# Kernel optimization log

Measured on AMD Instinct MI355X. Metric: run time of the kernel, lower is better.

The kernel has to match this reference:

```python
import jax, jax.numpy as jnp
import numpy as np
from jax import lax


def _conv(x, w, pad):
    # NCHW / OIHW conv, stride 1
    return lax.conv_general_dilated(
        x, w, window_strides=(1, 1), padding=((pad, pad), (pad, pad)),
        dimension_numbers=("NCHW", "OIHW", "NCHW"))


def setup_inputs() -> dict:
    key = jax.random.key(0)
    k1, k2, k3, k4 = jax.random.split(key, 4)
    B, C, H, W = 16, 64, 128, 128
    OUT = 64
    x = jax.random.normal(k1, (B, C, H, W), jnp.float32)
    w_off = jax.random.normal(k2, (2 * C, C, 3, 3), jnp.float32) * 0.01  # offset conv, init std 0.01
    w_conv = jax.random.normal(k3, (OUT, C, 3, 3), jnp.float32) * 0.05
    b_conv = jax.random.normal(k4, (OUT,), jnp.float32) * 0.01
    return {"x": x, "w_off": w_off, "w_conv": w_conv, "b_conv": b_conv}


def _deform(x, w_off):
    B, C, H, W = x.shape
    off = _conv(x, w_off, 1)                      # (B, 2C, H, W)
    # Faithful to torch .view(-1, H, W, 2): raw row-major memory reinterpretation
    off = off.reshape(B * C, H * W, 2)            # (BC, HW, 2) -> (row_off, col_off)
    gr, gc = jnp.meshgrid(jnp.arange(H), jnp.arange(W), indexing="ij")
    grid = jnp.stack([gr.reshape(-1), gc.reshape(-1)], -1).astype(x.dtype)  # (HW, 2)
    coords = off + grid                           # (BC, HW, 2)
    rows = jnp.clip(coords[..., 0], 0, H - 1)
    cols = jnp.clip(coords[..., 1], 0, W - 1)
    r0 = jnp.floor(rows); r1 = jnp.ceil(rows)
    c0 = jnp.floor(cols); c1 = jnp.ceil(cols)
    xf = x.reshape(B * C, H * W)

    def gather(r, c):
        idx = lax.stop_gradient((r * W + c).astype(jnp.int32))
        return jnp.take_along_axis(xf, idx, axis=1)

    v_lt = gather(r0, c0)   # (floor row, floor col)
    v_rb = gather(r1, c1)   # (ceil row,  ceil col)
    v_lb = gather(r0, c1)   # (floor row, ceil col)
    v_rt = gather(r1, c0)   # (ceil row,  floor col)
    fr = rows - r0
    fc = cols - c0
    vals_t = fr * (v_rt - v_lt) + v_lt
    vals_b = fr * (v_rb - v_lb) + v_lb
    mapped = fc * (vals_b - vals_t) + vals_t      # (BC, HW)
    return mapped.reshape(B, C, H, W)


def reference(x, w_off, w_conv, b_conv):
    xd = _deform(x, w_off)
    return _conv(xd, w_conv, 1) + b_conv[None, :, None, None]
```

## Files before the change

kernel.cpp:

```cpp
#include <hip/hip_runtime.h>

typedef _Float16 f16;
typedef _Float16 half8 __attribute__((ext_vector_type(8)));
typedef _Float16 f16x2 __attribute__((ext_vector_type(2)));
typedef float f32x4 __attribute__((ext_vector_type(4)));
typedef int i32x4 __attribute__((ext_vector_type(4)));
typedef unsigned short ushort_t;


__global__ __launch_bounds__(256) void pack_w_k(
    const float* __restrict__ w_off, const float* __restrict__ w_conv,
    f16* __restrict__ W1p, f16* __restrict__ W2p)
{
    int t = blockIdx.x * 256 + threadIdx.x;
    if (t < 73728) {
        int tap = t >> 13, oc = (t >> 6) & 127, ic = t & 63;
        W1p[t] = (f16)w_off[(oc * 64 + ic) * 9 + tap];
    } else {
        int t2 = t - 73728;
        int tap = t2 >> 12, oc = (t2 >> 6) & 63, ic = t2 & 63;
        W2p[t2] = (f16)w_conv[(oc * 64 + ic) * 9 + tap];
    }
}

__global__ __launch_bounds__(256) void transpose_k(
    const float* __restrict__ x, f16* __restrict__ xT)
{
    __shared__ float lds[64 * 132];
    const int b = blockIdx.x >> 7, h = blockIdx.x & 127;
    const int tid = threadIdx.x;
    const float4* x4 = (const float4*)x;
    for (int i = tid; i < 2048; i += 256) {
        int ic = i >> 5, wq = i & 31;
        float4 v = x4[(b * 64 + ic) * 4096 + h * 32 + wq];
        *(float4*)&lds[ic * 132 + wq * 4] = v;
    }
    __syncthreads();
    for (int i = tid; i < 1024; i += 256) {
        int w = i & 127, kg = i >> 7;
        half8 hv;
        #pragma unroll
        for (int j = 0; j < 8; ++j) hv[j] = (f16)lds[(kg * 8 + j) * 132 + w];
        *(half8*)&xT[(((size_t)(b * 128 + h) * 128 + w) << 6) + kg * 8] = hv;
    }
}

__device__ __forceinline__ float bilin(const float* __restrict__ xp, float rr, float cc) {
    rr = fminf(fmaxf(rr, 0.f), 127.f);
    cc = fminf(fmaxf(cc, 0.f), 127.f);
    const float r0f = floorf(rr), c0f = floorf(cc);
    const float r1f = ceilf(rr),  c1f = ceilf(cc);
    const int r0 = (int)r0f, r1 = (int)r1f, c0 = (int)c0f, c1 = (int)c1f;
    const float v_lt = xp[(r0 << 7) + c0];
    const float v_rt = xp[(r1 << 7) + c0];
    const float v_lb = xp[(r0 << 7) + c1];
    const float v_rb = xp[(r1 << 7) + c1];
    const float fr = rr - r0f, fc = cc - c0f;
    const float vt = fr * (v_rt - v_lt) + v_lt;
    const float vb = fr * (v_rb - v_lb) + v_lb;
    return fc * (vb - vt) + vt;
}

__global__ __launch_bounds__(256, 2) void conv1_deform_k(
    const f16* __restrict__ xT, const float* __restrict__ x,
    const f16* __restrict__ Wp, f16* __restrict__ mapped)
{
    __shared__ char lds[66560];
    ushort_t* cres = (ushort_t*)lds;

    const int tid = threadIdx.x;
    const int t = blockIdx.x;
    const int b = blockIdx.y;

    {
        const i32x4* s4 = (const i32x4*)xT;
        for (int s = tid; s < 4160; s += 256) {
            int kg = s & 7, q = s >> 3;
            int c = q % 130, r = q / 130;
            int rowg = 2 * t + r - 1, wg = c - 1;
            i32x4 v = {0, 0, 0, 0};
            if ((unsigned)rowg < 128u && (unsigned)wg < 128u)
                v = s4[((b * 128 + rowg) * 128 + wg) * 8 + kg];
            int off = (q << 7) + (kg << 4);
            off ^= (c & 7) << 4;
            *(i32x4*)(lds + off) = v;
        }
    }
    __syncthreads();

    const int lane = tid & 63, wv = tid >> 6;
    const int l15 = lane & 15, l4 = lane >> 4;
    const int wm = wv >> 1, u = wv & 1;
    const int ocbA = wm * 64 + l15;

    f32x4 acc[4][8];
    #pragma unroll
    for (int m = 0; m < 4; ++m)
        #pragma unroll
        for (int n = 0; n < 8; ++n) acc[m][n] = {0.f, 0.f, 0.f, 0.f};

    half8 a_cur[4], a_nxt[4];
    #pragma unroll
    for (int m = 0; m < 4; ++m)
        a_cur[m] = *(const half8*)&Wp[(0 * 128 + ocbA + m * 16) * 64 + l4 * 8];

    #pragma unroll
    for (int step = 0; step < 18; ++step) {
        const int tap = step >> 1, ks = step & 1;
        const int ky = tap / 3, kx = tap % 3;
        if (step < 17) {
            const int tap1 = (step + 1) >> 1, ks1 = (step + 1) & 1;
            #pragma unroll
            for (int m = 0; m < 4; ++m)
                a_nxt[m] = *(const half8*)&Wp[(tap1 * 128 + ocbA + m * 16) * 64 + ks1 * 32 + l4 * 8];
        }
        half8 bf[8];
        #pragma unroll
        for (int n = 0; n < 8; ++n) {
            const int c = n * 16 + l15 + kx;
            int off = (((u + ky) * 130 + c) << 7) + (ks << 6) + (l4 << 4);
            off ^= (c & 7) << 4;
            bf[n] = *(const half8*)(lds + off);
        }
        #pragma unroll
        for (int m = 0; m < 4; ++m)
            #pragma unroll
            for (int n = 0; n < 8; ++n)
                acc[m][n] = __builtin_amdgcn_mfma_f32_16x16x32_f16(
                    a_cur[m], bf[n], acc[m][n], 0, 0, 0);
        #pragma unroll
        for (int m = 0; m < 4; ++m) a_cur[m] = a_nxt[m];
    }

    __syncthreads();

    #pragma unroll
    for (int m = 0; m < 4; ++m) {
        const int oc0 = wm * 64 + m * 16 + l4 * 4;
        #pragma unroll
        for (int n = 0; n < 8; ++n) {
            const int w = n * 16 + l15;
            const int base = (u * 128 + w) * 130 + oc0;
            f16x2 p0; p0[0] = (f16)acc[m][n][0]; p0[1] = (f16)acc[m][n][1];
            f16x2 p1; p1[0] = (f16)acc[m][n][2]; p1[1] = (f16)acc[m][n][3];
            *(f16x2*)&cres[base]     = p0;
            *(f16x2*)&cres[base + 2] = p1;
        }
    }
    __syncthreads();

    {
        const int half_ = wv & 1;
        const int w_out = half_ * 64 + lane;
        const int wq = 2 * lane;
        const int c0 = (wv >> 1) * 32;
        const size_t mbase = ((size_t)b << 14);

        #pragma unroll 4
        for (int cc = 0; cc < 32; ++cc) {
            const int c = c0 + cc;
            const f16x2 R = *(const f16x2*)&cres[(half_ * 128 + wq) * 130 + 2 * c];
            const f16x2 Cf = *(const f16x2*)&cres[(half_ * 128 + wq + 1) * 130 + 2 * c];
            const float* xp = x + (((size_t)b * 64 + c) << 14);
            const float v0 = bilin(xp, (float)R[0] + (float)t,        (float)Cf[0] + (float)w_out);
            const float v1 = bilin(xp, (float)R[1] + (float)(t + 64), (float)Cf[1] + (float)w_out);
            mapped[(mbase + (size_t)t * 128 + w_out) * 64 + c]          = (f16)v0;
            mapped[(mbase + (size_t)(t + 64) * 128 + w_out) * 64 + c]   = (f16)v1;
        }
    }
}

__global__ __launch_bounds__(256, 2) void conv2_k(
    const f16* __restrict__ src, const f16* __restrict__ Wp,
    const float* __restrict__ bias, float* __restrict__ out)
{
    __shared__ char lds[66560];
    const int tid = threadIdx.x;
    const int s = blockIdx.x;
    const int b = blockIdx.y;

    {
        const i32x4* s4 = (const i32x4*)src;
        for (int i = tid; i < 4160; i += 256) {
            int kg = i & 7, q = i >> 3;
            int c = q % 130, r = q / 130;
            int rowg = 2 * s + r - 1, wg = c - 1;
            i32x4 v = {0, 0, 0, 0};
            if ((unsigned)rowg < 128u && (unsigned)wg < 128u)
                v = s4[((b * 128 + rowg) * 128 + wg) * 8 + kg];
            int off = (q << 7) + (kg << 4);
            off ^= (c & 7) << 4;
            *(i32x4*)(lds + off) = v;
        }
    }
    __syncthreads();

    const int lane = tid & 63, wv = tid >> 6;
    const int l15 = lane & 15, l4 = lane >> 4;
    const int u = wv >> 1, pixb = (wv & 1) * 64;

    f32x4 acc[4][4];
    #pragma unroll
    for (int m = 0; m < 4; ++m)
        #pragma unroll
        for (int n = 0; n < 4; ++n) acc[m][n] = {0.f, 0.f, 0.f, 0.f};

    half8 ab[3][4];
    #pragma unroll
    for (int m = 0; m < 4; ++m) {
        ab[0][m] = *(const half8*)&Wp[(0 * 64 + l15 + m * 16) * 64 + 0 * 32 + l4 * 8];
        ab[1][m] = *(const half8*)&Wp[(0 * 64 + l15 + m * 16) * 64 + 1 * 32 + l4 * 8];
    }

    #pragma unroll
    for (int step = 0; step < 18; ++step) {
        const int tap = step >> 1, ks = step & 1;
        const int ky = tap / 3, kx = tap % 3;
        if (step < 16) {
            const int tap2 = (step + 2) >> 1, ks2 = (step + 2) & 1;
            #pragma unroll
            for (int m = 0; m < 4; ++m)
                ab[(step + 2) % 3][m] =
                    *(const half8*)&Wp[(tap2 * 64 + l15 + m * 16) * 64 + ks2 * 32 + l4 * 8];
        }
        half8 bf[4];
        #pragma unroll
        for (int n = 0; n < 4; ++n) {
            const int c = pixb + n * 16 + l15 + kx;
            int off = (((u + ky) * 130 + c) << 7) + (ks << 6) + (l4 << 4);
            off ^= (c & 7) << 4;
            bf[n] = *(const half8*)(lds + off);
        }
        #pragma unroll
        for (int m = 0; m < 4; ++m)
            #pragma unroll
            for (int n = 0; n < 4; ++n)
                acc[m][n] = __builtin_amdgcn_mfma_f32_16x16x32_f16(
                    ab[step % 3][m], bf[n], acc[m][n], 0, 0, 0);
    }

    const int orow = 2 * s + u;
    #pragma unroll
    for (int m = 0; m < 4; ++m) {
        #pragma unroll
        for (int i = 0; i < 4; ++i) {
            const int oc = m * 16 + l4 * 4 + i;
            const float bb = bias[oc];
            #pragma unroll
            for (int n = 0; n < 4; ++n) {
                const int pix = pixb + n * 16 + l15;
                out[(((size_t)b * 64 + oc) << 14) + orow * 128 + pix] = acc[m][n][i] + bb;
            }
        }
    }
}

extern "C" void kernel_launch(void* const* d_in, const int* in_sizes, int n_in,
                              void* d_out, int out_size, void* d_ws, size_t ws_size,
                              hipStream_t stream) {
    const float* x      = (const float*)d_in[0];
    const float* w_off  = (const float*)d_in[1];
    const float* w_conv = (const float*)d_in[2];
    const float* b_conv = (const float*)d_in[3];
    float* out = (float*)d_out;

    char* ws = (char*)d_ws;
    f16* xT     = (f16*)ws;
    f16* mapped = (f16*)(ws + 33554432);
    f16* W1p    = (f16*)(ws + 67108864);
    f16* W2p    = (f16*)(ws + 67108864 + 147456);

    pack_w_k<<<432, 256, 0, stream>>>(w_off, w_conv, W1p, W2p);
    transpose_k<<<2048, 256, 0, stream>>>(x, xT);
    conv1_deform_k<<<dim3(64, 16), 256, 0, stream>>>(xT, x, W1p, mapped);
    conv2_k<<<dim3(64, 16), 256, 0, stream>>>(mapped, W2p, b_conv, out);
}
```

Measured before the change: 311.2 us.

## Halve per-block tile to one row, raise occupancy, vectorize deform stores

Both conv kernels now process one output row per block instead of two, which doubles the grid, shrinks LDS from 66560 to 49920 bytes and cuts the accumulator count so launch bounds can allow three blocks per CU. Warps are re-split over output channels, and each LDS B-fragment is consumed right away by two MFMAs instead of being buffered. The deform epilogue is rewritten so each thread gathers 8 channels and writes them as one 16-byte half8 store, replacing scattered 2-byte stores. In exchange, the halo rows are reloaded more often relative to useful rows, and weight loads are repeated across twice as many blocks.

Result: faster. 271.6 us (-12.7%).

```diff
diff --git a/kernel.cpp b/kernel.cpp
--- a/kernel.cpp
+++ b/kernel.cpp
@@ -61,23 +61,24 @@
     return fc * (vb - vt) + vt;
 }
 
-__global__ __launch_bounds__(256, 2) void conv1_deform_k(
+__global__ __launch_bounds__(256, 3) void conv1_deform_k(
     const f16* __restrict__ xT, const float* __restrict__ x,
     const f16* __restrict__ Wp, f16* __restrict__ mapped)
 {
-    __shared__ char lds[66560];
+    __shared__ char lds[49920];
     ushort_t* cres = (ushort_t*)lds;
 
     const int tid = threadIdx.x;
-    const int t = blockIdx.x;
+    const int sr = blockIdx.x;
     const int b = blockIdx.y;
+    const int t = sr >> 1, u = sr & 1;
 
     {
         const i32x4* s4 = (const i32x4*)xT;
-        for (int s = tid; s < 4160; s += 256) {
+        for (int s = tid; s < 3120; s += 256) {
             int kg = s & 7, q = s >> 3;
             int c = q % 130, r = q / 130;
-            int rowg = 2 * t + r - 1, wg = c - 1;
+            int rowg = sr + r - 1, wg = c - 1;
             i32x4 v = {0, 0, 0, 0};
             if ((unsigned)rowg < 128u && (unsigned)wg < 128u)
                 v = s4[((b * 128 + rowg) * 128 + wg) * 8 + kg];
@@ -90,19 +91,18 @@
 
     const int lane = tid & 63, wv = tid >> 6;
     const int l15 = lane & 15, l4 = lane >> 4;
-    const int wm = wv >> 1, u = wv & 1;
-    const int ocbA = wm * 64 + l15;
-
-    f32x4 acc[4][8];
-    #pragma unroll
-    for (int m = 0; m < 4; ++m)
+    const int ocb = wv * 32 + l15;
+
+    f32x4 acc[2][8];
+    #pragma unroll
+    for (int m = 0; m < 2; ++m)
         #pragma unroll
         for (int n = 0; n < 8; ++n) acc[m][n] = {0.f, 0.f, 0.f, 0.f};
 
-    half8 a_cur[4], a_nxt[4];
-    #pragma unroll
-    for (int m = 0; m < 4; ++m)
-        a_cur[m] = *(const half8*)&Wp[(0 * 128 + ocbA + m * 16) * 64 + l4 * 8];
+    half8 a_cur[2], a_nxt[2];
+    #pragma unroll
+    for (int m = 0; m < 2; ++m)
+        a_cur[m] = *(const half8*)&Wp[(0 * 128 + ocb + m * 16) * 64 + l4 * 8];
 
     #pragma unroll
     for (int step = 0; step < 18; ++step) {
@@ -111,36 +111,31 @@
         if (step < 17) {
             const int tap1 = (step + 1) >> 1, ks1 = (step + 1) & 1;
             #pragma unroll
-            for (int m = 0; m < 4; ++m)
-                a_nxt[m] = *(const half8*)&Wp[(tap1 * 128 + ocbA + m * 16) * 64 + ks1 * 32 + l4 * 8];
-        }
-        half8 bf[8];
+            for (int m = 0; m < 2; ++m)
+                a_nxt[m] = *(const half8*)&Wp[(tap1 * 128 + ocb + m * 16) * 64 + ks1 * 32 + l4 * 8];
+        }
         #pragma unroll
         for (int n = 0; n < 8; ++n) {
             const int c = n * 16 + l15 + kx;
-            int off = (((u + ky) * 130 + c) << 7) + (ks << 6) + (l4 << 4);
-            off ^= (c & 7) << 4;
-            bf[n] = *(const half8*)(lds + off);
-        }
-        #pragma unroll
-        for (int m = 0; m < 4; ++m)
-            #pragma unroll
-            for (int n = 0; n < 8; ++n)
-                acc[m][n] = __builtin_amdgcn_mfma_f32_16x16x32_f16(
-                    a_cur[m], bf[n], acc[m][n], 0, 0, 0);
-        #pragma unroll
-        for (int m = 0; m < 4; ++m) a_cur[m] = a_nxt[m];
-    }
-
-    __syncthreads();
-
-    #pragma unroll
-    for (int m = 0; m < 4; ++m) {
-        const int oc0 = wm * 64 + m * 16 + l4 * 4;
+            int off = ((ky * 130 + c) << 7) + (ks << 6) + (l4 << 4);
+            off ^= (c & 7) << 4;
+            const half8 bf = *(const half8*)(lds + off);
+            acc[0][n] = __builtin_amdgcn_mfma_f32_16x16x32_f16(a_cur[0], bf, acc[0][n], 0, 0, 0);
+            acc[1][n] = __builtin_amdgcn_mfma_f32_16x16x32_f16(a_cur[1], bf, acc[1][n], 0, 0, 0);
+        }
+        #pragma unroll
+        for (int m = 0; m < 2; ++m) a_cur[m] = a_nxt[m];
+    }
+
+    __syncthreads();
+
+    #pragma unroll
+    for (int m = 0; m < 2; ++m) {
+        const int oc0 = wv * 32 + m * 16 + l4 * 4;
         #pragma unroll
         for (int n = 0; n < 8; ++n) {
-            const int w = n * 16 + l15;
-            const int base = (u * 128 + w) * 130 + oc0;
+            const int pix = n * 16 + l15;
+            const int base = pix * 130 + oc0;
             f16x2 p0; p0[0] = (f16)acc[m][n][0]; p0[1] = (f16)acc[m][n][1];
             f16x2 p1; p1[0] = (f16)acc[m][n][2]; p1[1] = (f16)acc[m][n][3];
             *(f16x2*)&cres[base]     = p0;
@@ -150,41 +145,46 @@
     __syncthreads();
 
     {
-        const int half_ = wv & 1;
-        const int w_out = half_ * 64 + lane;
-        const int wq = 2 * lane;
-        const int c0 = (wv >> 1) * 32;
-        const size_t mbase = ((size_t)b << 14);
-
-        #pragma unroll 4
-        for (int cc = 0; cc < 32; ++cc) {
-            const int c = c0 + cc;
-            const f16x2 R = *(const f16x2*)&cres[(half_ * 128 + wq) * 130 + 2 * c];
-            const f16x2 Cf = *(const f16x2*)&cres[(half_ * 128 + wq + 1) * 130 + 2 * c];
-            const float* xp = x + (((size_t)b * 64 + c) << 14);
-            const float v0 = bilin(xp, (float)R[0] + (float)t,        (float)Cf[0] + (float)w_out);
-            const float v1 = bilin(xp, (float)R[1] + (float)(t + 64), (float)Cf[1] + (float)w_out);
-            mapped[(mbase + (size_t)t * 128 + w_out) * 64 + c]          = (f16)v0;
-            mapped[(mbase + (size_t)(t + 64) * 128 + w_out) * 64 + c]   = (f16)v1;
-        }
-    }
-}
-
-__global__ __launch_bounds__(256, 2) void conv2_k(
+        const int hsel = tid >> 7;
+        const int c0 = ((tid >> 6) & 1) * 32;
+        const int w_off = tid & 63;
+        const int w_out = u * 64 + w_off;
+        const int h_out = t + hsel * 64;
+        const int wq = 2 * w_off;
+        const float hb = (float)h_out, wb = (float)w_out;
+        f16* mp = mapped + ((((size_t)b << 14) + h_out * 128 + w_out) << 6) + c0;
+
+        #pragma unroll
+        for (int j = 0; j < 4; ++j) {
+            half8 ov;
+            #pragma unroll
+            for (int e = 0; e < 8; ++e) {
+                const int c = c0 + j * 8 + e;
+                const float R  = (float)*(const f16*)&cres[wq * 130 + 2 * c + hsel];
+                const float Cf = (float)*(const f16*)&cres[(wq + 1) * 130 + 2 * c + hsel];
+                const float* xp = x + (((size_t)b * 64 + c) << 14);
+                ov[e] = (f16)bilin(xp, R + hb, Cf + wb);
+            }
+            *(half8*)&mp[j * 8] = ov;
+        }
+    }
+}
+
+__global__ __launch_bounds__(256, 3) void conv2_k(
     const f16* __restrict__ src, const f16* __restrict__ Wp,
     const float* __restrict__ bias, float* __restrict__ out)
 {
-    __shared__ char lds[66560];
+    __shared__ char lds[49920];
     const int tid = threadIdx.x;
-    const int s = blockIdx.x;
+    const int h = blockIdx.x;
     const int b = blockIdx.y;
 
     {
         const i32x4* s4 = (const i32x4*)src;
-        for (int i = tid; i < 4160; i += 256) {
-            int kg = i & 7, q = i >> 3;
+        for (int s = tid; s < 3120; s += 256) {
+            int kg = s & 7, q = s >> 3;
             int c = q % 130, r = q / 130;
-            int rowg = 2 * s + r - 1, wg = c - 1;
+            int rowg = h + r - 1, wg = c - 1;
             i32x4 v = {0, 0, 0, 0};
             if ((unsigned)rowg < 128u && (unsigned)wg < 128u)
                 v = s4[((b * 128 + rowg) * 128 + wg) * 8 + kg];
@@ -197,59 +197,54 @@
 
     const int lane = tid & 63, wv = tid >> 6;
     const int l15 = lane & 15, l4 = lane >> 4;
-    const int u = wv >> 1, pixb = (wv & 1) * 64;
-
-    f32x4 acc[4][4];
-    #pragma unroll
-    for (int m = 0; m < 4; ++m)
+    const int wm = wv >> 1, wn = wv & 1;
+    const int ocb = wm * 32 + l15;
+    const int pixb = wn * 64;
+
+    f32x4 acc[2][4];
+    #pragma unroll
+    for (int m = 0; m < 2; ++m)
         #pragma unroll
         for (int n = 0; n < 4; ++n) acc[m][n] = {0.f, 0.f, 0.f, 0.f};
 
-    half8 ab[3][4];
-    #pragma unroll
-    for (int m = 0; m < 4; ++m) {
-        ab[0][m] = *(const half8*)&Wp[(0 * 64 + l15 + m * 16) * 64 + 0 * 32 + l4 * 8];
-        ab[1][m] = *(const half8*)&Wp[(0 * 64 + l15 + m * 16) * 64 + 1 * 32 + l4 * 8];
-    }
+    half8 a_cur[2], a_nxt[2];
+    #pragma unroll
+    for (int m = 0; m < 2; ++m)
+        a_cur[m] = *(const half8*)&Wp[(0 * 64 + ocb + m * 16) * 64 + l4 * 8];
 
     #pragma unroll
     for (int step = 0; step < 18; ++step) {
         const int tap = step >> 1, ks = step & 1;
         const int ky = tap / 3, kx = tap % 3;
-        if (step < 16) {
-            const int tap2 = (step + 2) >> 1, ks2 = (step + 2) & 1;
-            #pragma unroll
-            for (int m = 0; m < 4; ++m)
-                ab[(step + 2) % 3][m] =
-                    *(const half8*)&Wp[(tap2 * 64 + l15 + m * 16) * 64 + ks2 * 32 + l4 * 8];
-        }
-        half8 bf[4];
+        if (step < 17) {
+            const int tap1 = (step + 1) >> 1, ks1 = (step + 1) & 1;
+            #pragma unroll
+            for (int m = 0; m < 2; ++m)
+                a_nxt[m] = *(const half8*)&Wp[(tap1 * 64 + ocb + m * 16) * 64 + ks1 * 32 + l4 * 8];
+        }
         #pragma unroll
         for (int n = 0; n < 4; ++n) {
             const int c = pixb + n * 16 + l15 + kx;
-            int off = (((u + ky) * 130 + c) << 7) + (ks << 6) + (l4 << 4);
-            off ^= (c & 7) << 4;
-            bf[n] = *(const half8*)(lds + off);
-        }
-        #pragma unroll
-        for (int m = 0; m < 4; ++m)
-            #pragma unroll
-            for (int n = 0; n < 4; ++n)
-                acc[m][n] = __builtin_amdgcn_mfma_f32_16x16x32_f16(
-                    ab[step % 3][m], bf[n], acc[m][n], 0, 0, 0);
-    }
-
-    const int orow = 2 * s + u;
-    #pragma unroll
-    for (int m = 0; m < 4; ++m) {
+            int off = ((ky * 130 + c) << 7) + (ks << 6) + (l4 << 4);
+            off ^= (c & 7) << 4;
+            const half8 bf = *(const half8*)(lds + off);
+            acc[0][n] = __builtin_amdgcn_mfma_f32_16x16x32_f16(a_cur[0], bf, acc[0][n], 0, 0, 0);
+            acc[1][n] = __builtin_amdgcn_mfma_f32_16x16x32_f16(a_cur[1], bf, acc[1][n], 0, 0, 0);
+        }
+        #pragma unroll
+        for (int m = 0; m < 2; ++m) a_cur[m] = a_nxt[m];
+    }
+
+    #pragma unroll
+    for (int m = 0; m < 2; ++m) {
         #pragma unroll
         for (int i = 0; i < 4; ++i) {
-            const int oc = m * 16 + l4 * 4 + i;
+            const int oc = wm * 32 + m * 16 + l4 * 4 + i;
             const float bb = bias[oc];
             #pragma unroll
             for (int n = 0; n < 4; ++n) {
                 const int pix = pixb + n * 16 + l15;
-                out[(((size_t)b * 64 + oc) << 14) + orow * 128 + pix] = acc[m][n][i] + bb;
+                out[(((size_t)b * 64 + oc) << 14) + h * 128 + pix] = acc[m][n][i] + bb;
             }
         }
     }
@@ -272,6 +267,6 @@
 
     pack_w_k<<<432, 256, 0, stream>>>(w_off, w_conv, W1p, W2p);
     transpose_k<<<2048, 256, 0, stream>>>(x, xT);
-    conv1_deform_k<<<dim3(64, 16), 256, 0, stream>>>(xT, x, W1p, mapped);
-    conv2_k<<<dim3(64, 16), 256, 0, stream>>>(mapped, W2p, b_conv, out);
-}
+    conv1_deform_k<<<dim3(128, 16), 256, 0, stream>>>(xT, x, W1p, mapped);
+    conv2_k<<<dim3(128, 16), 256, 0, stream>>>(mapped, W2p, b_conv, out);
+}
```
